# Optimization experiments

Measured on AMD Instinct MI355X. Metric: run time of the kernel, lower is better.

Reference implementation:

```python
import jax, jax.numpy as jnp
import numpy as np

B, SC, ST = 16, 512, 512
DP, DC = 256, 128
D = DP + 2 * DC          # 512 = d_model
H, L, DFF = 8, 2, 2048
NCAT, NCONT = 1000, 2048


def sin_embed(vals, d, scale=1000.0):
    # vectorized sinusoidal_time_embedding: even dims -> sin(angle), odd dims -> cos(angle)
    i = jnp.arange(d, dtype=jnp.float32)
    ang = vals.astype(jnp.float32)[..., None] / jnp.power(scale, i / d)
    return jnp.where(i % 2 == 0, jnp.sin(ang), jnp.cos(ang))


def layer_norm(x, g, b, eps=1e-5):
    m = jnp.mean(x, -1, keepdims=True)
    v = jnp.mean(jnp.square(x - m), -1, keepdims=True)
    return (x - m) / jnp.sqrt(v + eps) * g + b


def setup_inputs() -> dict:
    key = jax.random.key(0)
    ks = jax.random.split(key, 16)
    s = 0.02
    def n(k, shape, scale=s):
        return jax.random.normal(k, shape, dtype=jnp.float32) * scale
    return {
        "context_cat": jax.random.randint(ks[0], (B, SC), 0, NCAT),
        "context_time": jax.random.uniform(ks[1], (B, SC), dtype=jnp.float32) * 100.0,
        "context_f0": jax.random.uniform(ks[2], (B, SC), dtype=jnp.float32) * 500.0,
        "target_cat": jax.random.randint(ks[3], (B, ST), 0, NCAT),
        "target_time": jax.random.uniform(ks[4], (B, ST), dtype=jnp.float32) * 100.0,
        "target_f0": jax.random.uniform(ks[5], (B, ST), dtype=jnp.float32) * 500.0,
        "cat_table": n(ks[6], (NCAT, DP), 1.0),
        "cont_table": sin_embed(jnp.arange(NCONT, dtype=jnp.float32), DC),  # frozen sin table
        "pad_emb": n(ks[7], (D,), 1.0),
        "Wq": n(ks[8], (L, D, D)), "bq": jnp.zeros((L, D)),
        "Wk": n(ks[9], (L, D, D)), "bk": jnp.zeros((L, D)),
        "Wv": n(ks[10], (L, D, D)), "bv": jnp.zeros((L, D)),
        "Wo": n(ks[11], (L, D, D)), "bo": jnp.zeros((L, D)),
        "ln1g": jnp.ones((L, D)), "ln1b": jnp.zeros((L, D)),
        "ln2g": jnp.ones((L, D)), "ln2b": jnp.zeros((L, D)),
        "W1": n(ks[12], (L, D, DFF)), "b1": jnp.zeros((L, DFF)),
        "W2": n(ks[13], (L, DFF, D)), "b2": jnp.zeros((L, D)),
    }


def reference(context_cat, context_time, context_f0, target_cat, target_time, target_f0,
              cat_table, cont_table, pad_emb,
              Wq, bq, Wk, bk, Wv, bv, Wo, bo,
              ln1g, ln1b, ln2g, ln2b, W1, b1, W2, b2):
    def embed(cat, tm, f0):
        pad = cat < 0
        e = jnp.concatenate(
            [cat_table[jnp.maximum(cat, 0)], sin_embed(tm, DC), sin_embed(f0, DC)], axis=-1)
        return jnp.where(pad[..., None], pad_emb, e), pad

    ce, cp = embed(context_cat, context_time, context_f0)
    te, tp = embed(target_cat, target_time, target_f0)
    x = jnp.concatenate([ce, te], axis=1)                       # [B, SC+ST, D]
    bias = jnp.where(jnp.concatenate([cp, tp], 1), -1e9, 0.0)[:, None, None, :]
    hd = D // H
    inv_sqrt = 1.0 / np.sqrt(hd).astype(np.float32)

    def step(h, p):
        wq, bq_, wk, bk_, wv, bv_, wo, bo_, g1, c1, g2, c2, w1, d1, w2, d2 = p
        Bn, S, _ = h.shape
        q = (h @ wq + bq_).reshape(Bn, S, H, hd)
        k = (h @ wk + bk_).reshape(Bn, S, H, hd)
        v = (h @ wv + bv_).reshape(Bn, S, H, hd)
        scores = jnp.einsum('bqhd,bkhd->bhqk', q, k) * inv_sqrt + bias
        attn = jax.nn.softmax(scores, axis=-1)
        o = jnp.einsum('bhqk,bkhd->bqhd', attn, v).reshape(Bn, S, D)
        h = layer_norm(h + o @ wo + bo_, g1, c1)                # post-norm (torch default)
        f = jax.nn.relu(h @ w1 + d1) @ w2 + d2
        return layer_norm(h + f, g2, c2), None

    x, _ = jax.lax.scan(step, x, (Wq, bq, Wk, bk, Wv, bv, Wo, bo,
                                  ln1g, ln1b, ln2g, ln2b, W1, b1, W2, b2))
    out = x[:, SC:, :]
    pred_cat = out[..., :DP] @ cat_table.T
    pred_time = out[..., DP:DP + DC] @ cont_table.T
    pred_f0 = out[..., DP + DC:] @ cont_table.T
    return pred_cat, pred_time, pred_f0
```

## Files before the change

kernel.cpp:

```cpp
#include <hip/hip_runtime.h>


typedef _Float16 half8 __attribute__((ext_vector_type(8)));
typedef _Float16 half4 __attribute__((ext_vector_type(4)));
typedef float f32x4 __attribute__((ext_vector_type(4)));

__device__ __forceinline__ void gl2lds16(const _Float16* g, _Float16* l) {
    __builtin_amdgcn_global_load_lds(
        (const __attribute__((address_space(1))) void*)g,
        (__attribute__((address_space(3))) void*)l, 16, 0, 0);
}

__global__ void cast_f32_f16_k(const float* __restrict__ in, _Float16* __restrict__ out,
                               long nsrc, long ntot) {
    long i = (long)blockIdx.x * blockDim.x + threadIdx.x;
    long stride = (long)gridDim.x * blockDim.x;
    for (; i < ntot; i += stride) out[i] = i < nsrc ? (_Float16)in[i] : (_Float16)0.f;
}

__global__ void tcast_k(const float* __restrict__ in, _Float16* __restrict__ out,
                        int R, int C, long zs, int rowoff) {
    __shared__ float tile[32][33];
    long z = blockIdx.z;
    const float* src = in + z * (long)R * C;
    _Float16* dst = out + z * zs + (long)rowoff * R;
    int c0 = blockIdx.x * 32, r0 = blockIdx.y * 32;
    for (int i = threadIdx.y; i < 32; i += 8)
        tile[i][threadIdx.x] = src[(long)(r0 + i) * C + c0 + threadIdx.x];
    __syncthreads();
    for (int i = threadIdx.y; i < 32; i += 8)
        dst[(long)(c0 + i) * R + r0 + threadIdx.x] = (_Float16)tile[threadIdx.x][i];
}

__global__ void bcat_k(const float* __restrict__ bq, const float* __restrict__ bk,
                       const float* __restrict__ bv, float* __restrict__ out, int L) {
    int i = blockIdx.x * 256 + threadIdx.x;
    if (i >= L * 1536) return;
    int l = i / 1536, j = i - l * 1536;
    float v = j < 512 ? bq[l * 512 + j] : (j < 1024 ? bk[l * 512 + j - 512] : bv[l * 512 + j - 1024]);
    out[i] = v;
}

__global__ void vtrans_k(const _Float16* __restrict__ qkv, _Float16* __restrict__ vT) {
    __shared__ _Float16 tile[32][33];
    int bh = blockIdx.z; int b = bh >> 3, h = bh & 7;
    int s0 = blockIdx.x * 32, d0 = blockIdx.y * 32;
    const _Float16* src = qkv + ((long)b * 1024) * 1536 + 1024 + h * 64;
    _Float16* dst = vT + (long)bh * 64 * 1024;
    for (int i = threadIdx.y; i < 32; i += 8)
        tile[i][threadIdx.x] = src[(long)(s0 + i) * 1536 + d0 + threadIdx.x];
    __syncthreads();
    for (int i = threadIdx.y; i < 32; i += 8)
        dst[(long)(d0 + i) * 1024 + s0 + threadIdx.x] = tile[threadIdx.x][i];
}

__global__ __launch_bounds__(128) void embed_k(
    const int* __restrict__ ccat, const float* __restrict__ ctime, const float* __restrict__ cf0,
    const int* __restrict__ tcat, const float* __restrict__ ttime, const float* __restrict__ tf0,
    const float* __restrict__ cat_table, const float* __restrict__ pad_emb,
    float* __restrict__ xf, _Float16* __restrict__ xb, float* __restrict__ biasKey) {
    int t = blockIdx.x;
    int b = t >> 10, s = t & 1023;
    int j = b * 512 + (s & 511);
    int cat; float tm, f0;
    if (s < 512) { cat = ccat[j]; tm = ctime[j]; f0 = cf0[j]; }
    else         { cat = tcat[j]; tm = ttime[j]; f0 = tf0[j]; }
    bool pad = cat < 0;
    if (threadIdx.x == 0) biasKey[t] = pad ? -1e9f : 0.f;
    int c = cat < 0 ? 0 : cat;
    #pragma unroll
    for (int u = 0; u < 4; u++) {
        int d = threadIdx.x * 4 + u;
        float val;
        if (pad) val = pad_emb[d];
        else if (d < 256) val = cat_table[(long)c * 256 + d];
        else {
            float base = (d < 384) ? tm : f0;
            int i = (d < 384) ? (d - 256) : (d - 384);
            float ang = base / powf(1000.f, (float)i * (1.f / 128.f));
            val = (i & 1) ? cosf(ang) : sinf(ang);
        }
        long o = (long)t * 512 + d;
        xf[o] = val;
        xb[o] = (_Float16)val;
    }
}

__global__ __launch_bounds__(256) void layernorm_k(
    float* xf, _Float16* __restrict__ xb,
    const float* __restrict__ g, const float* __restrict__ beta) {
    long row = blockIdx.x;
    int tid = threadIdx.x;
    float* xr = xf + row * 512;
    float v0 = xr[tid], v1 = xr[tid + 256];
    float s = v0 + v1, q = v0 * v0 + v1 * v1;
    #pragma unroll
    for (int o = 32; o; o >>= 1) { s += __shfl_down(s, o); q += __shfl_down(q, o); }
    __shared__ float rs[4], rq[4];
    if ((tid & 63) == 0) { rs[tid >> 6] = s; rq[tid >> 6] = q; }
    __syncthreads();
    s = rs[0] + rs[1] + rs[2] + rs[3];
    q = rq[0] + rq[1] + rq[2] + rq[3];
    float mean = s * (1.f / 512.f);
    float var = q * (1.f / 512.f) - mean * mean;
    float rstd = rsqrtf(var + 1e-5f);
    float y0 = (v0 - mean) * rstd * g[tid] + beta[tid];
    float y1 = (v1 - mean) * rstd * g[tid + 256] + beta[tid + 256];
    xr[tid] = y0; xr[tid + 256] = y1;
    xb[row * 512 + tid] = (_Float16)y0;
    xb[row * 512 + tid + 256] = (_Float16)y1;
}

__global__ __launch_bounds__(256, 3) void flash_k(
    const _Float16* __restrict__ QKV, const _Float16* __restrict__ VT,
    const float* __restrict__ biasKey, _Float16* __restrict__ O) {
    const int S = 1024, D = 512, LDQ = 1536, NT = 16;
    int bh = blockIdx.x; int b = bh >> 3, h = bh & 7;
    int qt = blockIdx.y;
    int tid = threadIdx.x, w = tid >> 6, lane = tid & 63;
    int g = lane >> 4, q15 = lane & 15;

    __shared__ __align__(16) _Float16 Ks[2][64 * 64];
    __shared__ __align__(16) _Float16 VTs[2][64 * 64];
    __shared__ __align__(16) _Float16 Ps[4][16][72];
    __shared__ __align__(16) float biasLds[1024];

    {
        const float* bsrc = biasKey + (long)b * S;
        f32x4 bv4 = *(const f32x4*)&bsrc[tid * 4];
        #pragma unroll
        for (int r = 0; r < 4; r++) bv4[r] *= 1.442695041f;
        *(f32x4*)&biasLds[tid * 4] = bv4;
    }

    int qrow = qt * 64 + w * 16 + q15;
    const _Float16* qp = QKV + ((long)(b * S + qrow)) * LDQ + h * 64 + g * 8;
    half8 qf[2];
    qf[0] = *(const half8*)(qp);
    qf[1] = *(const half8*)(qp + 32);
    const _Float16 qsc = (_Float16)0.1803368801f;
    #pragma unroll
    for (int kk = 0; kk < 2; kk++)
        #pragma unroll
        for (int i = 0; i < 8; i++) qf[kk][i] *= qsc;

    const _Float16* kbase = QKV + 512 + ((long)b * S) * LDQ + h * 64;
    const _Float16* vbase = VT + (long)bh * 64 * S;

    auto stage = [&](int buf, int kt) {
        #pragma unroll
        for (int i = 0; i < 2; i++) {
            int c = tid + i * 256;
            int row = c >> 3, p = c & 7;
            int s = p ^ (row & 7);
            gl2lds16(kbase + (long)(kt * 64 + row) * LDQ + s * 8, &Ks[buf][c * 8]);
            gl2lds16(vbase + (long)row * S + kt * 64 + s * 8, &VTs[buf][c * 8]);
        }
    };

    f32x4 acc_o[4];
    #pragma unroll
    for (int i = 0; i < 4; i++)
        #pragma unroll
        for (int r = 0; r < 4; r++) acc_o[i][r] = 0.f;
    float m_run = -1e30f, l_run = 0.f;

    stage(0, 0);
    int cur = 0;
    for (int kt = 0; kt < NT; kt++) {
        __syncthreads();
        if (kt + 1 < NT) stage(cur ^ 1, kt + 1);

        f32x4 acc[4];
        #pragma unroll
        for (int mf = 0; mf < 4; mf++)
            #pragma unroll
            for (int r = 0; r < 4; r++) acc[mf][r] = 0.f;
        __builtin_amdgcn_s_setprio(1);
        #pragma unroll
        for (int kk = 0; kk < 2; kk++)
            #pragma unroll
            for (int mf = 0; mf < 4; mf++) {
                int row = mf * 16 + q15;
                half8 kf = *(const half8*)&Ks[cur][row * 64 + (((kk * 4 + g) ^ (row & 7)) * 8)];
                acc[mf] = __builtin_amdgcn_mfma_f32_16x16x32_f16(kf, qf[kk], acc[mf], 0, 0, 0);
            }
        __builtin_amdgcn_s_setprio(0);

        float mt = -1e30f;
        #pragma unroll
        for (int mf = 0; mf < 4; mf++) {
            f32x4 b4 = *(const f32x4*)&biasLds[kt * 64 + mf * 16 + g * 4];
            #pragma unroll
            for (int r = 0; r < 4; r++) {
                float sv = acc[mf][r] + b4[r];
                acc[mf][r] = sv;
                mt = fmaxf(mt, sv);
            }
        }
        mt = fmaxf(mt, __shfl_xor(mt, 16));
        mt = fmaxf(mt, __shfl_xor(mt, 32));

        float rsum = 0.f;
        if (__all((int)(mt - m_run <= 8.f))) {
            #pragma unroll
            for (int mf = 0; mf < 4; mf++)
                #pragma unroll
                for (int r = 0; r < 4; r++) {
                    float p = exp2f(acc[mf][r] - m_run);
                    acc[mf][r] = p; rsum += p;
                }
        } else {
            float m_new = fmaxf(m_run, mt);
            float scale = exp2f(m_run - m_new);
            #pragma unroll
            for (int mf = 0; mf < 4; mf++)
                #pragma unroll
                for (int r = 0; r < 4; r++) {
                    float p = exp2f(acc[mf][r] - m_new);
                    acc[mf][r] = p; rsum += p;
                }
            float sc[4];
            #pragma unroll
            for (int r = 0; r < 4; r++) sc[r] = __shfl(scale, g * 4 + r);
            #pragma unroll
            for (int nf = 0; nf < 4; nf++)
                #pragma unroll
                for (int r = 0; r < 4; r++) acc_o[nf][r] *= sc[r];
            l_run *= scale;
            m_run = m_new;
        }
        rsum += __shfl_xor(rsum, 16);
        rsum += __shfl_xor(rsum, 32);
        l_run += rsum;

        #pragma unroll
        for (int mf = 0; mf < 4; mf++) {
            half4 h4;
            #pragma unroll
            for (int r = 0; r < 4; r++) h4[r] = (_Float16)acc[mf][r];
            *(half4*)&Ps[w][q15][mf * 16 + g * 4] = h4;
        }

        __builtin_amdgcn_s_setprio(1);
        #pragma unroll
        for (int kk = 0; kk < 2; kk++) {
            half8 pa = *(const half8*)&Ps[w][q15][kk * 32 + g * 8];
            #pragma unroll
            for (int nf = 0; nf < 4; nf++) {
                int row = nf * 16 + q15;
                half8 vf = *(const half8*)&VTs[cur][row * 64 + (((kk * 4 + g) ^ (row & 7)) * 8)];
                acc_o[nf] = __builtin_amdgcn_mfma_f32_16x16x32_f16(pa, vf, acc_o[nf], 0, 0, 0);
            }
        }
        __builtin_amdgcn_s_setprio(0);
        cur ^= 1;
    }

    float linv = 1.f / l_run;
    float lv[4];
    #pragma unroll
    for (int r = 0; r < 4; r++) lv[r] = __shfl(linv, g * 4 + r);
    _Float16* obase = O + ((long)(b * S + qt * 64 + w * 16)) * D + h * 64;
    #pragma unroll
    for (int nf = 0; nf < 4; nf++)
        #pragma unroll
        for (int r = 0; r < 4; r++) {
            int row = g * 4 + r;
            obase[(long)row * D + nf * 16 + q15] = (_Float16)(acc_o[nf][r] * lv[r]);
        }
}

__global__ __launch_bounds__(256) void gemm_nt(
    const _Float16* __restrict__ A, long lda, long sA1, long sA2,
    const _Float16* __restrict__ Bm, long ldb, long sB1, long sB2,
    float* Cf, _Float16* Cb, long ldc, long sC1, long sC2,
    const float* __restrict__ bias, long sb1, long sb2,
    const float* resid,
    int M, int N, int K, int Z2, float alpha, int relu) {
    int z = blockIdx.z;
    int z1 = z / Z2, z2 = z - z1 * Z2;
    A  += z1 * sA1 + z2 * sA2;
    Bm += z1 * sB1 + z2 * sB2;
    long coff = z1 * sC1 + z2 * sC2;
    if (bias) bias += z1 * sb1 + z2 * sb2;

    int gx = gridDim.x;
    int nwg = gx * gridDim.y;
    int bid = blockIdx.y * gx + blockIdx.x;
    int q = nwg >> 3, r = nwg & 7;
    int xcd = bid & 7, ii = bid >> 3;
    int swz = (xcd < r ? xcd * (q + 1) : r * (q + 1) + (xcd - r) * q) + ii;
    int m0 = (swz / gx) * 128;
    int n0 = (swz % gx) * 128;

    __shared__ __align__(16) _Float16 As[2][128 * 32];
    __shared__ __align__(16) _Float16 Bs[2][128 * 32];

    int tid = threadIdx.x;
    int lane = tid & 63;
    int w = tid >> 6;
    int wr = (w >> 1) << 6;
    int wc = (w & 1) << 6;

    f32x4 acc[4][4];
    #pragma unroll
    for (int i = 0; i < 4; i++)
        #pragma unroll
        for (int jj = 0; jj < 4; jj++) { acc[i][jj][0] = 0.f; acc[i][jj][1] = 0.f; acc[i][jj][2] = 0.f; acc[i][jj][3] = 0.f; }

    int fr = lane & 15;
    int g = lane >> 4;
    int rs8 = (g ^ (fr & 3)) * 8;

    auto stage = [&](int buf, int kt) {
        #pragma unroll
        for (int i = 0; i < 2; i++) {
            int idx = tid + i * 256;
            int row = idx >> 2, s = idx & 3;
            int sg = s ^ (row & 3);
            gl2lds16(A + (long)(m0 + row) * lda + kt * 32 + sg * 8, &As[buf][idx * 8]);
            gl2lds16(Bm + (long)(n0 + row) * ldb + kt * 32 + sg * 8, &Bs[buf][idx * 8]);
        }
    };

    int nk = K >> 5;
    stage(0, 0);
    __syncthreads();

    int cur = 0;
    for (int kt = 0; kt < nk; kt++) {
        if (kt + 1 < nk) stage(cur ^ 1, kt + 1);
        half8 af[4], bfv[4];
        #pragma unroll
        for (int m = 0; m < 4; m++) af[m] = *(const half8*)&As[cur][(wr + m * 16 + fr) * 32 + rs8];
        #pragma unroll
        for (int n = 0; n < 4; n++) bfv[n] = *(const half8*)&Bs[cur][(wc + n * 16 + fr) * 32 + rs8];
        #pragma unroll
        for (int m = 0; m < 4; m++)
            #pragma unroll
            for (int n = 0; n < 4; n++)
                acc[m][n] = __builtin_amdgcn_mfma_f32_16x16x32_f16(af[m], bfv[n], acc[m][n], 0, 0, 0);
        __syncthreads();
        cur ^= 1;
    }

    int fq = lane >> 4;
    #pragma unroll
    for (int m = 0; m < 4; m++) {
        #pragma unroll
        for (int jj = 0; jj < 4; jj++) {
            long row = m0 + wr + m * 16 + fq * 4 + jj;
            #pragma unroll
            for (int n = 0; n < 4; n++) {
                int col = n0 + wc + n * 16 + fr;
                if (col < N) {
                    float v = acc[m][n][jj] * alpha;
                    if (bias) v += bias[col];
                    long o = coff + row * ldc + col;
                    if (resid) v += resid[o];
                    if (relu) v = fmaxf(v, 0.f);
                    if (Cf) Cf[o] = v;
                    if (Cb) Cb[o] = (_Float16)v;
                }
            }
        }
    }
}

extern "C" void kernel_launch(void* const* d_in, const int* in_sizes, int n_in,
                              void* d_out, int out_size, void* d_ws, size_t ws_size,
                              hipStream_t stream) {
    const int Bn = 16, S = 1024, D = 512, H = 8, L = 2, DFF = 2048, NCAT = 1000, NCONT = 2048;
    const long M = (long)Bn * S;

    const int*   ccat      = (const int*)d_in[0];
    const float* ctime     = (const float*)d_in[1];
    const float* cf0       = (const float*)d_in[2];
    const int*   tcat      = (const int*)d_in[3];
    const float* ttime     = (const float*)d_in[4];
    const float* tf0       = (const float*)d_in[5];
    const float* cat_table = (const float*)d_in[6];
    const float* cont_tab  = (const float*)d_in[7];
    const float* pad_emb   = (const float*)d_in[8];
    const float* Wq = (const float*)d_in[9];
    const float* bq = (const float*)d_in[10];
    const float* Wk = (const float*)d_in[11];
    const float* bk = (const float*)d_in[12];
    const float* Wv = (const float*)d_in[13];
    const float* bv = (const float*)d_in[14];
    const float* Wo = (const float*)d_in[15];
    const float* bo = (const float*)d_in[16];
    const float* ln1g = (const float*)d_in[17];
    const float* ln1b = (const float*)d_in[18];
    const float* ln2g = (const float*)d_in[19];
    const float* ln2b = (const float*)d_in[20];
    const float* W1 = (const float*)d_in[21];
    const float* b1 = (const float*)d_in[22];
    const float* W2 = (const float*)d_in[23];
    const float* b2 = (const float*)d_in[24];

    char* wsb = (char*)d_ws;
    size_t off = 0;
    auto alloc = [&](size_t bytes) -> void* {
        off = (off + 255) & ~(size_t)255;
        void* p = wsb + off; off += bytes; return p;
    };

    float*     xf      = (float*)alloc(M * D * 4);
    _Float16*  xb      = (_Float16*)alloc(M * D * 2);
    _Float16*  qkv     = (_Float16*)alloc(M * 3 * D * 2);
    _Float16*  vT      = (_Float16*)alloc(M * D * 2);
    _Float16*  ob      = (_Float16*)alloc(M * D * 2);
    float*     biasKey = (float*)alloc(M * 4);
    _Float16*  WqkvT = (_Float16*)alloc((size_t)L * 3 * D * D * 2);
    float*     bqkv  = (float*)alloc((size_t)L * 3 * D * 4);
    _Float16*  WoT  = (_Float16*)alloc((size_t)L * D * D * 2);
    _Float16*  W1T  = (_Float16*)alloc((size_t)L * D * DFF * 2);
    _Float16*  W2T  = (_Float16*)alloc((size_t)L * DFF * D * 2);
    _Float16*  catT = (_Float16*)alloc((size_t)1024 * 256 * 2);
    _Float16*  conT = (_Float16*)alloc((size_t)NCONT * 128 * 2);

    size_t need_ffh = (size_t)M * DFF * 2;
    _Float16* ffh;
    size_t offAl = (off + 255) & ~(size_t)255;
    if (offAl + need_ffh <= ws_size) ffh = (_Float16*)alloc(need_ffh);
    else ffh = (_Float16*)d_out;

    auto gemm = [&](const _Float16* A, long lda, long sA1, long sA2,
                    const _Float16* Bm, long ldb, long sB1, long sB2,
                    float* Cf, _Float16* Cb, long ldc, long sC1, long sC2,
                    const float* bias, long sb1, long sb2,
                    const float* resid, int Mm, int Nn, int Kk,
                    int Z1, int Z2, float alpha, int relu) {
        dim3 gdim((Nn + 127) / 128, (Mm + 127) / 128, Z1 * Z2);
        gemm_nt<<<gdim, 256, 0, stream>>>(A, lda, sA1, sA2, Bm, ldb, sB1, sB2,
                                          Cf, Cb, ldc, sC1, sC2, bias, sb1, sb2,
                                          resid, Mm, Nn, Kk, Z2, alpha, relu);
    };

    dim3 tb(32, 8);
    tcast_k<<<dim3(D / 32, D / 32, L), tb, 0, stream>>>(Wq, WqkvT, D, D, (long)3 * D * D, 0);
    tcast_k<<<dim3(D / 32, D / 32, L), tb, 0, stream>>>(Wk, WqkvT, D, D, (long)3 * D * D, D);
    tcast_k<<<dim3(D / 32, D / 32, L), tb, 0, stream>>>(Wv, WqkvT, D, D, (long)3 * D * D, 2 * D);
    bcat_k<<<dim3((L * 1536 + 255) / 256), 256, 0, stream>>>(bq, bk, bv, bqkv, L);
    tcast_k<<<dim3(D / 32, D / 32, L), tb, 0, stream>>>(Wo, WoT, D, D, (long)D * D, 0);
    tcast_k<<<dim3(DFF / 32, D / 32, L), tb, 0, stream>>>(W1, W1T, D, DFF, (long)D * DFF, 0);
    tcast_k<<<dim3(D / 32, DFF / 32, L), tb, 0, stream>>>(W2, W2T, DFF, D, (long)DFF * D, 0);
    cast_f32_f16_k<<<dim3(512), 256, 0, stream>>>(cat_table, catT, (long)NCAT * 256, (long)1024 * 256);
    cast_f32_f16_k<<<dim3(512), 256, 0, stream>>>(cont_tab, conT, (long)NCONT * 128, (long)NCONT * 128);

    embed_k<<<dim3((unsigned)M), 128, 0, stream>>>(ccat, ctime, cf0, tcat, ttime, tf0,
                                                   cat_table, pad_emb, xf, xb, biasKey);

    for (int l = 0; l < L; l++) {
        gemm(xb, D, 0, 0, WqkvT + (size_t)l * 3 * D * D, D, 0, 0, nullptr, qkv, 3 * D, 0, 0,
             bqkv + (size_t)l * 3 * D, 0, 0, nullptr, (int)M, 3 * D, D, 1, 1, 1.f, 0);
        vtrans_k<<<dim3(32, 2, Bn * H), tb, 0, stream>>>(qkv, vT);

        flash_k<<<dim3(Bn * H, S / 64), 256, 0, stream>>>(qkv, vT, biasKey, ob);

        gemm(ob, D, 0, 0, WoT + (size_t)l * D * D, D, 0, 0, xf, nullptr, D, 0, 0,
             bo + l * D, 0, 0, xf, (int)M, D, D, 1, 1, 1.f, 0);
        layernorm_k<<<dim3((unsigned)M), 256, 0, stream>>>(xf, xb, ln1g + l * D, ln1b + l * D);

        gemm(xb, D, 0, 0, W1T + (size_t)l * D * DFF, D, 0, 0, nullptr, ffh, DFF, 0, 0,
             b1 + l * DFF, 0, 0, nullptr, (int)M, DFF, D, 1, 1, 1.f, 1);
        gemm(ffh, DFF, 0, 0, W2T + (size_t)l * DFF * D, DFF, 0, 0, xf, nullptr, D, 0, 0,
             b2 + l * D, 0, 0, xf, (int)M, D, DFF, 1, 1, 1.f, 0);
        layernorm_k<<<dim3((unsigned)M), 256, 0, stream>>>(xf, xb, ln2g + l * D, ln2b + l * D);
    }

    float* out_cat  = (float*)d_out;
    float* out_time = out_cat + (size_t)Bn * 512 * NCAT;
    float* out_f0   = out_time + (size_t)Bn * 512 * NCONT;
    gemm(xb + (size_t)512 * D, D, (long)S * D, 0,
         catT, 256, 0, 0,
         out_cat, nullptr, NCAT, (long)512 * NCAT, 0,
         nullptr, 0, 0, nullptr, 512, NCAT, 256, Bn, 1, 1.f, 0);
    gemm(xb + (size_t)512 * D + 256, D, (long)S * D, 0,
         conT, 128, 0, 0,
         out_time, nullptr, NCONT, (long)512 * NCONT, 0,
         nullptr, 0, 0, nullptr, 512, NCONT, 128, Bn, 1, 1.f, 0);
    gemm(xb + (size_t)512 * D + 384, D, (long)S * D, 0,
         conT, 128, 0, 0,
         out_f0, nullptr, NCONT, (long)512 * NCONT, 0,
         nullptr, 0, 0, nullptr, 512, NCONT, 128, Bn, 1, 1.f, 0);
}
```

Measured before the change: 921.1 us.

## Software-pipeline attention QK ahead of softmax and triple-buffer GEMM loads

The attention kernel splits K and V staging and computes the next tile's QK^T scores while the current tile's softmax and PV run, alternating two score register sets so MFMA work overlaps the exp/max VALU work. The GEMM moves from double to triple buffering with explicit vmcnt waits and a single barrier per k-step, keeping two tiles of loads in flight. This adds register pressure in attention and more LDS in the GEMM, which may lower occupancy. The explicit vmcnt counts rely on each stage issuing exactly four loads per thread.

```diff
diff --git a/kernel.cpp b/kernel.cpp
--- a/kernel.cpp
+++ b/kernel.cpp
@@ -147,13 +147,21 @@
     const _Float16* kbase = QKV + 512 + ((long)b * S) * LDQ + h * 64;
     const _Float16* vbase = VT + (long)bh * 64 * S;
 
-    auto stage = [&](int buf, int kt) {
+    auto stageK = [&](int buf, int kt) {
         #pragma unroll
         for (int i = 0; i < 2; i++) {
             int c = tid + i * 256;
             int row = c >> 3, p = c & 7;
             int s = p ^ (row & 7);
             gl2lds16(kbase + (long)(kt * 64 + row) * LDQ + s * 8, &Ks[buf][c * 8]);
+        }
+    };
+    auto stageV = [&](int buf, int kt) {
+        #pragma unroll
+        for (int i = 0; i < 2; i++) {
+            int c = tid + i * 256;
+            int row = c >> 3, p = c & 7;
+            int s = p ^ (row & 7);
             gl2lds16(vbase + (long)row * S + kt * 64 + s * 8, &VTs[buf][c * 8]);
         }
     };
@@ -165,36 +173,33 @@
         for (int r = 0; r < 4; r++) acc_o[i][r] = 0.f;
     float m_run = -1e30f, l_run = 0.f;
 
-    stage(0, 0);
-    int cur = 0;
-    for (int kt = 0; kt < NT; kt++) {
-        __syncthreads();
-        if (kt + 1 < NT) stage(cur ^ 1, kt + 1);
-
-        f32x4 acc[4];
+    auto QK = [&](int kt, f32x4 (&s)[4]) {
         #pragma unroll
         for (int mf = 0; mf < 4; mf++)
             #pragma unroll
-            for (int r = 0; r < 4; r++) acc[mf][r] = 0.f;
+            for (int r = 0; r < 4; r++) s[mf][r] = 0.f;
+        int buf = kt & 1;
         __builtin_amdgcn_s_setprio(1);
         #pragma unroll
         for (int kk = 0; kk < 2; kk++)
             #pragma unroll
             for (int mf = 0; mf < 4; mf++) {
                 int row = mf * 16 + q15;
-                half8 kf = *(const half8*)&Ks[cur][row * 64 + (((kk * 4 + g) ^ (row & 7)) * 8)];
-                acc[mf] = __builtin_amdgcn_mfma_f32_16x16x32_f16(kf, qf[kk], acc[mf], 0, 0, 0);
+                half8 kf = *(const half8*)&Ks[buf][row * 64 + (((kk * 4 + g) ^ (row & 7)) * 8)];
+                s[mf] = __builtin_amdgcn_mfma_f32_16x16x32_f16(kf, qf[kk], s[mf], 0, 0, 0);
             }
         __builtin_amdgcn_s_setprio(0);
-
+    };
+
+    auto SMPV = [&](int kt, f32x4 (&s)[4]) {
         float mt = -1e30f;
         #pragma unroll
         for (int mf = 0; mf < 4; mf++) {
             f32x4 b4 = *(const f32x4*)&biasLds[kt * 64 + mf * 16 + g * 4];
             #pragma unroll
             for (int r = 0; r < 4; r++) {
-                float sv = acc[mf][r] + b4[r];
-                acc[mf][r] = sv;
+                float sv = s[mf][r] + b4[r];
+                s[mf][r] = sv;
                 mt = fmaxf(mt, sv);
             }
         }
@@ -202,13 +207,13 @@
         mt = fmaxf(mt, __shfl_xor(mt, 32));
 
         float rsum = 0.f;
-        if (__all((int)(mt - m_run <= 8.f))) {
+        if (__all(mt - m_run <= 8.f)) {
             #pragma unroll
             for (int mf = 0; mf < 4; mf++)
                 #pragma unroll
                 for (int r = 0; r < 4; r++) {
-                    float p = exp2f(acc[mf][r] - m_run);
-                    acc[mf][r] = p; rsum += p;
+                    float p = exp2f(s[mf][r] - m_run);
+                    s[mf][r] = p; rsum += p;
                 }
         } else {
             float m_new = fmaxf(m_run, mt);
@@ -217,8 +222,8 @@
             for (int mf = 0; mf < 4; mf++)
                 #pragma unroll
                 for (int r = 0; r < 4; r++) {
-                    float p = exp2f(acc[mf][r] - m_new);
-                    acc[mf][r] = p; rsum += p;
+                    float p = exp2f(s[mf][r] - m_new);
+                    s[mf][r] = p; rsum += p;
                 }
             float sc[4];
             #pragma unroll
@@ -238,10 +243,11 @@
         for (int mf = 0; mf < 4; mf++) {
             half4 h4;
             #pragma unroll
-            for (int r = 0; r < 4; r++) h4[r] = (_Float16)acc[mf][r];
+            for (int r = 0; r < 4; r++) h4[r] = (_Float16)s[mf][r];
             *(half4*)&Ps[w][q15][mf * 16 + g * 4] = h4;
         }
 
+        int buf = kt & 1;
         __builtin_amdgcn_s_setprio(1);
         #pragma unroll
         for (int kk = 0; kk < 2; kk++) {
@@ -249,12 +255,29 @@
             #pragma unroll
             for (int nf = 0; nf < 4; nf++) {
                 int row = nf * 16 + q15;
-                half8 vf = *(const half8*)&VTs[cur][row * 64 + (((kk * 4 + g) ^ (row & 7)) * 8)];
+                half8 vf = *(const half8*)&VTs[buf][row * 64 + (((kk * 4 + g) ^ (row & 7)) * 8)];
                 acc_o[nf] = __builtin_amdgcn_mfma_f32_16x16x32_f16(pa, vf, acc_o[nf], 0, 0, 0);
             }
         }
         __builtin_amdgcn_s_setprio(0);
-        cur ^= 1;
+    };
+
+    f32x4 sA[4], sB[4];
+    stageK(0, 0); stageV(0, 0); stageK(1, 1);
+    __syncthreads();
+    QK(0, sA);
+
+    for (int t = 0; t < NT; t += 2) {
+        __syncthreads();
+        if (t + 2 < NT) stageK(t & 1, t + 2);
+        if (t + 1 < NT) stageV((t + 1) & 1, t + 1);
+        if (t + 1 < NT) QK(t + 1, sB);
+        SMPV(t, sA);
+        __syncthreads();
+        if (t + 3 < NT) stageK((t + 1) & 1, t + 3);
+        if (t + 2 < NT) stageV(t & 1, t + 2);
+        if (t + 2 < NT) QK(t + 2, sA);
+        SMPV(t + 1, sB);
     }
 
     float linv = 1.f / l_run;
@@ -294,8 +317,8 @@
     int m0 = (swz / gx) * 128;
     int n0 = (swz % gx) * 128;
 
-    __shared__ __align__(16) _Float16 As[2][128 * 32];
-    __shared__ __align__(16) _Float16 Bs[2][128 * 32];
+    __shared__ __align__(16) _Float16 As[3][128 * 32];
+    __shared__ __align__(16) _Float16 Bs[3][128 * 32];
 
     int tid = threadIdx.x;
     int lane = tid & 63;
@@ -326,11 +349,16 @@
 
     int nk = K >> 5;
     stage(0, 0);
-    __syncthreads();
-
-    int cur = 0;
-    for (int kt = 0; kt < nk; kt++) {
-        if (kt + 1 < nk) stage(cur ^ 1, kt + 1);
+    stage(1, 1);
+
+    for (int t = 0; t < nk; ++t) {
+        if (t + 1 < nk) asm volatile("s_waitcnt vmcnt(4)" ::: "memory");
+        else            asm volatile("s_waitcnt vmcnt(0)" ::: "memory");
+        __builtin_amdgcn_s_barrier();
+        __builtin_amdgcn_sched_barrier(0);
+        int cur = t % 3;
+        if (t + 2 < nk) stage((t + 2) % 3, t + 2);
+
         half8 af[4], bfv[4];
         #pragma unroll
         for (int m = 0; m < 4; m++) af[m] = *(const half8*)&As[cur][(wr + m * 16 + fr) * 32 + rs8];
@@ -341,8 +369,6 @@
             #pragma unroll
             for (int n = 0; n < 4; n++)
                 acc[m][n] = __builtin_amdgcn_mfma_f32_16x16x32_f16(af[m], bfv[n], acc[m][n], 0, 0, 0);
-        __syncthreads();
-        cur ^= 1;
     }
 
     int fq = lane >> 4;
```

After: 935.0 us. About the same (+1.5%).
